# Performance work log

Hardware: AMD Instinct MI355X
Metric: run time of the kernel (lower is better)

Reference implementation:

```python
import jax, jax.numpy as jnp
import numpy as np

NUM_NODES = 10000
IN_DIM = 128
GAT_UNITS = 64
K = 20  # min(20, num_nodes - 1)
NEG_SLOPE = 0.2


def setup_inputs() -> dict:
    key = jax.random.key(0)
    ks = jax.random.split(key, 10)
    s = lambda k, shape, scale: jax.random.normal(k, shape, jnp.float32) * scale
    return {
        "x": s(ks[0], (NUM_NODES, IN_DIM), 1.0),
        "emb": s(ks[1], (NUM_NODES, 16), 1.0),
        "W1": s(ks[2], (IN_DIM, 4, GAT_UNITS), 0.05),
        "a1_src": s(ks[3], (4, GAT_UNITS), 0.05),
        "a1_tgt": s(ks[4], (4, GAT_UNITS), 0.05),
        "b1": jnp.zeros((4 * GAT_UNITS,), jnp.float32),
        "W2": s(ks[5], (4 * GAT_UNITS, 1, GAT_UNITS), 0.05),
        "a2_src": s(ks[6], (1, GAT_UNITS), 0.05),
        "a2_tgt": s(ks[7], (1, GAT_UNITS), 0.05),
        "b2": jnp.zeros((GAT_UNITS,), jnp.float32),
    }


def _build_edges(emb):
    # top-k adjacency from cosine similarity of node embeddings
    norm = emb / jnp.linalg.norm(emb, axis=-1, keepdims=True)
    sim = norm @ norm.T                      # [N, N]
    _, idx = jax.lax.top_k(sim, K)           # [N, K]
    n = emb.shape[0]
    src = jnp.repeat(jnp.arange(n, dtype=jnp.int32), K)
    tgt = idx.reshape(-1).astype(jnp.int32)
    # append self loops (as in the original module)
    loop = jnp.arange(n, dtype=jnp.int32)
    src = jnp.concatenate([src, loop])
    tgt = jnp.concatenate([tgt, loop])
    return src, tgt                          # each [N*(K+1)]


def _gat(x, W, a_src, a_tgt, src, tgt, n):
    # x: [N, F]; W: [F, H, C]; a_*: [H, C]
    h = jnp.einsum("nf,fhc->nhc", x, W)      # [N, H, C]
    e_src = jnp.einsum("nhc,hc->nh", h, a_src)  # [N, H]
    e_tgt = jnp.einsum("nhc,hc->nh", h, a_tgt)  # [N, H]
    logits = jax.nn.leaky_relu(e_src[src] + e_tgt[tgt], NEG_SLOPE)  # [E, H]
    # segment softmax over each source node's neighborhood
    m = jax.ops.segment_max(logits, src, num_segments=n)
    ex = jnp.exp(logits - m[src])
    z = jax.ops.segment_sum(ex, src, num_segments=n)
    alpha = ex / z[src]                      # [E, H]
    msg = alpha[:, :, None] * h[tgt]         # [E, H, C]
    return jax.ops.segment_sum(msg, src, num_segments=n)  # [N, H, C]


def reference(x, emb, W1, a1_src, a1_tgt, b1, W2, a2_src, a2_tgt, b2):
    n = x.shape[0]
    src, tgt = _build_edges(emb)
    # GAT layer 1: 4 heads, concatenated
    h1 = _gat(x, W1, a1_src, a1_tgt, src, tgt, n)        # [N, 4, C]
    h1 = h1.reshape(n, -1) + b1                           # [N, 4C]
    h1 = jax.nn.relu(h1)                                  # (dropout: inference mode)
    # GAT layer 2: 1 head, no concat
    h2 = _gat(h1, W2, a2_src, a2_tgt, src, tgt, n)        # [N, 1, C]
    return h2[:, 0, :] + b2                               # [N, C]
```

## Files before the change

### kernel.cpp

```cpp
#include <hip/hip_runtime.h>
#include <math.h>


#define N_NODES 10000
#define EMB_D   16
#define IN_DIM  128
#define H1      4
#define CDIM    64
#define D1      256
#define K_TOP   20
#define NEIGH   21
#define SROWS   32
#define NTILES  313
#define JSPLIT  2
#define HALFT   160
#define CAPM    96
#define GUARD   0.016f

typedef __attribute__((ext_vector_type(8)))  short short8;
typedef __attribute__((ext_vector_type(16))) float f32x16;

__device__ __forceinline__ unsigned monokey(float v) {
  unsigned u = __float_as_uint(v);
  return (u & 0x80000000u) ? ~u : (u | 0x80000000u);
}
__device__ __forceinline__ float invmono(unsigned m) {
  unsigned u = (m & 0x80000000u) ? (m ^ 0x80000000u) : ~m;
  return __uint_as_float(u);
}
__device__ __forceinline__ unsigned short f32_to_bf16(float f) {
  unsigned u = __float_as_uint(f);
  unsigned r = 0x7FFFu + ((u >> 16) & 1u);
  return (unsigned short)((u + r) >> 16);
}

__device__ __forceinline__ float dot16q(float4 qa, float4 qb, float4 qc, float4 qd,
                                        float4 v0, float4 v1, float4 v2, float4 v3) {
  float a = 0.f;
  a = fmaf(qa.x, v0.x, a); a = fmaf(qa.y, v0.y, a);
  a = fmaf(qa.z, v0.z, a); a = fmaf(qa.w, v0.w, a);
  a = fmaf(qb.x, v1.x, a); a = fmaf(qb.y, v1.y, a);
  a = fmaf(qb.z, v1.z, a); a = fmaf(qb.w, v1.w, a);
  a = fmaf(qc.x, v2.x, a); a = fmaf(qc.y, v2.y, a);
  a = fmaf(qc.z, v2.z, a); a = fmaf(qc.w, v2.w, a);
  a = fmaf(qd.x, v3.x, a); a = fmaf(qd.y, v3.y, a);
  a = fmaf(qd.z, v3.z, a); a = fmaf(qd.w, v3.w, a);
  return a;
}

__global__ __launch_bounds__(256) void normalize_kernel(
    const float* __restrict__ emb, float* __restrict__ nrm,
    unsigned short* __restrict__ nrmh) {
  int i = blockIdx.x * 256 + threadIdx.x;
  if (i >= N_NODES) return;
  const float4* p = (const float4*)(emb + (size_t)i * EMB_D);
  float4 v[4];
  float ss = 0.f;
#pragma unroll
  for (int k = 0; k < 4; k++) {
    v[k] = p[k];
    ss = fmaf(v[k].x, v[k].x, ss);
    ss = fmaf(v[k].y, v[k].y, ss);
    ss = fmaf(v[k].z, v[k].z, ss);
    ss = fmaf(v[k].w, v[k].w, ss);
  }
  float nv = sqrtf(ss);
  float4* o = (float4*)(nrm + (size_t)i * EMB_D);
  ushort4* oh = (ushort4*)(nrmh + (size_t)i * EMB_D);
#pragma unroll
  for (int k = 0; k < 4; k++) {
    float4 t;
    t.x = v[k].x / nv; t.y = v[k].y / nv; t.z = v[k].z / nv; t.w = v[k].w / nv;
    o[k] = t;
    ushort4 h;
    h.x = f32_to_bf16(t.x); h.y = f32_to_bf16(t.y);
    h.z = f32_to_bf16(t.z); h.w = f32_to_bf16(t.w);
    oh[k] = h;
  }
}

__global__ __launch_bounds__(512) void sim_topk_part(
    const float* __restrict__ nrm, const unsigned short* __restrict__ nrmh,
    unsigned long long* __restrict__ pkeys) {
  __shared__ unsigned short s_qbf[SROWS * EMB_D];
  __shared__ float s_qf[SROWS * EMB_D];
  __shared__ __align__(16) char s_ovl[32768];
  float (*s_smax)[256] = (float(*)[256])s_ovl;
  unsigned long long (*s_ckey)[CAPM] = (unsigned long long(*)[CAPM])s_ovl;
  unsigned short (*s_cid)[CAPM] =
      (unsigned short(*)[CAPM])(s_ovl + 24576);
  __shared__ float s_thr[SROWS];
  __shared__ int s_cnt[SROWS];

  int tid = threadIdx.x;
  int w = tid >> 6, lane = tid & 63;
  int lo5 = lane & 31, hi = lane >> 5;
  int row0 = blockIdx.x * SROWS;
  int bh = blockIdx.y;
  int tbase = bh * HALFT;

  if (tid < SROWS * EMB_D) {
    int gi = row0 * EMB_D + tid;
    float v = (gi < N_NODES * EMB_D) ? nrm[gi] : 0.f;
    s_qf[tid] = v;
    s_qbf[tid] = f32_to_bf16(v);
  }
  if (tid < SROWS) s_cnt[tid] = 0;
  __syncthreads();

  short8 afrag = *(const short8*)&s_qbf[lo5 * EMB_D + hi * 8];
  const f32x16 zacc = (f32x16)0.0f;

  float rm[16];
#pragma unroll
  for (int r = 0; r < 16; r++) rm[r] = -INFINITY;

#pragma unroll
  for (int g = 0; g < 5; ++g) {
    int tb = tbase + g * 32 + w * 4;
    int nd[4];
    short8 bf[4];
#pragma unroll
    for (int u = 0; u < 4; u++) {
      nd[u] = (tb + u) * 32 + lo5;
      bf[u] = (short8)(short)0;
      if (nd[u] < N_NODES)
        bf[u] = *(const short8*)&nrmh[(size_t)nd[u] * EMB_D + hi * 8];
    }
#pragma unroll
    for (int u = 0; u < 4; u++) {
      f32x16 acc = __builtin_amdgcn_mfma_f32_32x32x16_bf16(afrag, bf[u], zacc, 0, 0, 0);
      if (nd[u] < N_NODES) {
#pragma unroll
        for (int r = 0; r < 16; r++) rm[r] = fmaxf(rm[r], acc[r]);
      }
    }
  }
#pragma unroll
  for (int r = 0; r < 16; r++) {
    int rl = (r & 3) + 8 * (r >> 2) + 4 * hi;
    s_smax[rl][w * 32 + lo5] = rm[r];
  }
  __syncthreads();

  for (int q = 0; q < 4; q++) {
    int row = w * 4 + q;
    float m01 = fmaxf(s_smax[row][lane], s_smax[row][64 + lane]);
    float m23 = fmaxf(s_smax[row][128 + lane], s_smax[row][192 + lane]);
    unsigned v = monokey(fmaxf(m01, m23));
#pragma unroll
    for (int k = 2; k <= 64; k <<= 1) {
#pragma unroll
      for (int j = k >> 1; j > 0; j >>= 1) {
        unsigned o = __shfl_xor(v, j);
        bool upper = (lane & j) != 0;
        bool ascend = (lane & k) == 0;
        unsigned mx = v > o ? v : o;
        unsigned mn = v > o ? o : v;
        v = (upper == ascend) ? mx : mn;
      }
    }
    unsigned t20 = __shfl(v, 44);
    if (lane == 0)
      s_thr[row] = (row0 + row < N_NODES) ? invmono(t20) - GUARD : INFINITY;
  }
  __syncthreads();

  float thr_r[16];
#pragma unroll
  for (int r = 0; r < 16; r++)
    thr_r[r] = s_thr[(r & 3) + 8 * (r >> 2) + 4 * hi];

#pragma unroll
  for (int g = 0; g < 5; ++g) {
    int tb = tbase + g * 32 + w * 4;
    int nd[4];
    short8 bf[4];
#pragma unroll
    for (int u = 0; u < 4; u++) {
      nd[u] = (tb + u) * 32 + lo5;
      bf[u] = (short8)(short)0;
      if (nd[u] < N_NODES)
        bf[u] = *(const short8*)&nrmh[(size_t)nd[u] * EMB_D + hi * 8];
    }
#pragma unroll
    for (int u = 0; u < 4; u++) {
      f32x16 acc = __builtin_amdgcn_mfma_f32_32x32x16_bf16(afrag, bf[u], zacc, 0, 0, 0);
      if (nd[u] < N_NODES) {
#pragma unroll
        for (int r = 0; r < 16; r++) {
          if (acc[r] >= thr_r[r]) {
            int rl = (r & 3) + 8 * (r >> 2) + 4 * hi;
            int slot = atomicAdd(&s_cnt[rl], 1);
            if (slot < CAPM) s_cid[rl][slot] = (unsigned short)nd[u];
          }
        }
      }
    }
  }
  __syncthreads();

  for (int q = 0; q < 4; q++) {
    int row = w * 4 + q;
    if (row0 + row >= N_NODES) continue;
    int M = s_cnt[row];
    if (M > CAPM) continue;
    const float4* qp = (const float4*)&s_qf[row * EMB_D];
    float4 qa = qp[0], qb = qp[1], qc = qp[2], qd = qp[3];
    for (int c = lane; c < M; c += 64) {
      int id = s_cid[row][c];
      const float4* pj = (const float4*)(nrm + (size_t)id * EMB_D);
      float sim = dot16q(qa, qb, qc, qd, pj[0], pj[1], pj[2], pj[3]);
      s_ckey[row][c] = ((unsigned long long)monokey(sim) << 32) |
                       (unsigned long long)(0xFFFFFFFFu - (unsigned)id);
    }
  }
  __syncthreads();

  for (int q = 0; q < 4; q++) {
    int row = w * 4 + q;
    int grow = row0 + row;
    if (grow >= N_NODES) continue;
    unsigned long long* outp = pkeys + ((size_t)grow * JSPLIT + bh) * K_TOP;
    int M = s_cnt[row];
    if (M <= CAPM) {
      for (int c = lane; c < M; c += 64) {
        unsigned long long mykey = s_ckey[row][c];
        int rank = 0;
        for (int i = 0; i < M; i++) rank += (s_ckey[row][i] > mykey) ? 1 : 0;
        if (rank < K_TOP) outp[rank] = mykey;
      }
    } else {
      const float4* qp = (const float4*)&s_qf[row * EMB_D];
      float4 qa = qp[0], qb = qp[1], qc = qp[2], qd = qp[3];
      int j0 = tbase * 32;
      int jend = j0 + HALFT * 32; if (jend > N_NODES) jend = N_NODES;
      unsigned long long prev = ~0ull;
      for (int r = 0; r < K_TOP; r++) {
        unsigned long long best = 0ull;
        for (int j = j0 + lane; j < jend; j += 64) {
          const float4* pj = (const float4*)(nrm + (size_t)j * EMB_D);
          float sim = dot16q(qa, qb, qc, qd, pj[0], pj[1], pj[2], pj[3]);
          unsigned long long key = ((unsigned long long)monokey(sim) << 32) |
                                   (unsigned long long)(0xFFFFFFFFu - (unsigned)j);
          if (key < prev && key > best) best = key;
        }
#pragma unroll
        for (int off = 32; off > 0; off >>= 1) {
          unsigned long long o = __shfl_down(best, off);
          if (o > best) best = o;
        }
        best = __shfl(best, 0);
        prev = best;
        if (lane == 0) outp[r] = best;
      }
    }
  }
}

__global__ __launch_bounds__(256) void topk_merge(
    const unsigned long long* __restrict__ pkeys, int* __restrict__ topk) {
  __shared__ unsigned long long s_k[4][JSPLIT * K_TOP];
  int w = threadIdx.x >> 6, lane = threadIdx.x & 63;
  int row = blockIdx.x * 4 + w;
  const unsigned long long* src = pkeys + (size_t)row * (JSPLIT * K_TOP);
  if (lane < JSPLIT * K_TOP) s_k[w][lane] = src[lane];
  __syncthreads();
  if (lane < JSPLIT * K_TOP) {
    unsigned long long mykey = s_k[w][lane];
    int rank = 0;
    for (int i = 0; i < JSPLIT * K_TOP; i++)
      rank += (s_k[w][i] > mykey) ? 1 : 0;
    if (rank < K_TOP)
      topk[(size_t)row * K_TOP + rank] =
          (int)(0xFFFFFFFFu - (unsigned)(mykey & 0xFFFFFFFFull));
  }
}

__global__ __launch_bounds__(512) void gemm1_kernel(
    const float* __restrict__ A, const float* __restrict__ B,
    const float* __restrict__ a_src, const float* __restrict__ a_tgt,
    float* __restrict__ Cc, float* __restrict__ es, float* __restrict__ et) {
  __shared__ float As[16][IN_DIM];
  int r0 = blockIdx.x * 16;
  int tid = threadIdx.y * 256 + threadIdx.x;
  {
    int rr = tid >> 5;
    int kk = tid & 31;
    ((float4*)&As[rr][0])[kk] = ((const float4*)(A + (size_t)(r0 + rr) * IN_DIM))[kk];
  }
  __syncthreads();
  int col = threadIdx.x;
  int y = threadIdx.y;
  float acc[8] = {0, 0, 0, 0, 0, 0, 0, 0};
  for (int k4 = 0; k4 < IN_DIM / 4; k4++) {
    float4 a[8];
#pragma unroll
    for (int r = 0; r < 8; r++) a[r] = ((const float4*)&As[y * 8 + r][0])[k4];
    float bv[4];
#pragma unroll
    for (int i = 0; i < 4; i++) bv[i] = B[(size_t)(k4 * 4 + i) * D1 + col];
#pragma unroll
    for (int r = 0; r < 8; r++) {
      acc[r] = fmaf(a[r].x, bv[0], acc[r]);
      acc[r] = fmaf(a[r].y, bv[1], acc[r]);
      acc[r] = fmaf(a[r].z, bv[2], acc[r]);
      acc[r] = fmaf(a[r].w, bv[3], acc[r]);
    }
  }
#pragma unroll
  for (int r = 0; r < 8; r++)
    Cc[(size_t)(r0 + y * 8 + r) * D1 + col] = acc[r];
  float as = a_src[col], at = a_tgt[col];
  int h = col >> 6;
#pragma unroll
  for (int r = 0; r < 8; r++) {
    float ps = acc[r] * as, pt = acc[r] * at;
#pragma unroll
    for (int off = 32; off > 0; off >>= 1) {
      ps += __shfl_down(ps, off);
      pt += __shfl_down(pt, off);
    }
    if ((col & 63) == 0) {
      es[(size_t)(r0 + y * 8 + r) * H1 + h] = ps;
      et[(size_t)(r0 + y * 8 + r) * H1 + h] = pt;
    }
  }
}

__global__ __launch_bounds__(256) void agg1_gemm2_kernel(
    const float* __restrict__ h1p, const float* __restrict__ e1s,
    const float* __restrict__ e1t, const int* __restrict__ topk,
    const float* __restrict__ b1, const float* __restrict__ B2,
    const float* __restrict__ a_src, const float* __restrict__ a_tgt,
    float* __restrict__ h2p, float* __restrict__ es, float* __restrict__ et) {
  __shared__ float As[16][D1];
  __shared__ int nb[16][NEIGH];
  __shared__ float wv[16][NEIGH][H1];
  __shared__ float zz[16][H1];
  int r0 = blockIdx.x * 16;
  int tid = threadIdx.x;

  for (int idx = tid; idx < 16 * NEIGH; idx += 256) {
    int n = idx / NEIGH, jj = idx % NEIGH;
    nb[n][jj] = (jj < K_TOP) ? topk[(size_t)(r0 + n) * K_TOP + jj] : (r0 + n);
  }
  __syncthreads();
  for (int idx = tid; idx < 16 * NEIGH * H1; idx += 256) {
    int e = idx & 3, jj = (idx >> 2) % NEIGH, n = idx / (NEIGH * H1);
    float L = e1s[(size_t)(r0 + n) * H1 + e] + e1t[(size_t)nb[n][jj] * H1 + e];
    wv[n][jj][e] = (L > 0.f) ? L : 0.2f * L;
  }
  __syncthreads();
  if (tid < 16 * H1) {
    int n = tid >> 2, h = tid & 3;
    float m = -INFINITY;
#pragma unroll
    for (int jj = 0; jj < NEIGH; jj++) m = fmaxf(m, wv[n][jj][h]);
    float z = 0.f;
#pragma unroll
    for (int jj = 0; jj < NEIGH; jj++) {
      float wt = expf(wv[n][jj][h] - m);
      z += wt;
      wv[n][jj][h] = wt;
    }
    zz[n][h] = z;
  }
  __syncthreads();
  {
    int h = tid >> 6;
    float bv = b1[tid];
    for (int n = 0; n < 16; n++) {
      float acc = 0.f;
#pragma unroll
      for (int jj = 0; jj < NEIGH; jj++)
        acc = fmaf(wv[n][jj][h], h1p[(size_t)nb[n][jj] * D1 + tid], acc);
      float o = acc / zz[n][h] + bv;
      As[n][tid] = fmaxf(o, 0.f);
    }
  }
  __syncthreads();
  int col = tid & 63, y = tid >> 6;
  float acc4[4] = {0, 0, 0, 0};
  for (int k4 = 0; k4 < D1 / 4; k4++) {
    float4 a[4];
#pragma unroll
    for (int r = 0; r < 4; r++) a[r] = ((const float4*)&As[y * 4 + r][0])[k4];
    float bv[4];
#pragma unroll
    for (int i = 0; i < 4; i++) bv[i] = B2[(size_t)(k4 * 4 + i) * CDIM + col];
#pragma unroll
    for (int r = 0; r < 4; r++) {
      acc4[r] = fmaf(a[r].x, bv[0], acc4[r]);
      acc4[r] = fmaf(a[r].y, bv[1], acc4[r]);
      acc4[r] = fmaf(a[r].z, bv[2], acc4[r]);
      acc4[r] = fmaf(a[r].w, bv[3], acc4[r]);
    }
  }
#pragma unroll
  for (int r = 0; r < 4; r++)
    h2p[(size_t)(r0 + y * 4 + r) * CDIM + col] = acc4[r];
  float as = a_src[col], at = a_tgt[col];
#pragma unroll
  for (int r = 0; r < 4; r++) {
    float ps = acc4[r] * as, pt = acc4[r] * at;
#pragma unroll
    for (int off = 32; off > 0; off >>= 1) {
      ps += __shfl_down(ps, off);
      pt += __shfl_down(pt, off);
    }
    if (col == 0) {
      es[r0 + y * 4 + r] = ps;
      et[r0 + y * 4 + r] = pt;
    }
  }
}

__global__ __launch_bounds__(256) void agg2_kernel(
    const float* __restrict__ h2p, const float* __restrict__ es,
    const float* __restrict__ et, const int* __restrict__ topk,
    const float* __restrict__ b2, float* __restrict__ out) {
  int tid = threadIdx.x;
  int li = tid >> 6;
  int c = tid & 63;
  int i = blockIdx.x * 4 + li;
  __shared__ int nb[4][NEIGH];
  __shared__ float lg[4][NEIGH];
  if (tid < 4 * NEIGH) {
    int li2 = tid / NEIGH, jj = tid % NEIGH;
    int node = blockIdx.x * 4 + li2;
    nb[li2][jj] = (jj < K_TOP) ? topk[(size_t)node * K_TOP + jj] : node;
  }
  __syncthreads();
  if (tid < 4 * NEIGH) {
    int li2 = tid / NEIGH, jj = tid % NEIGH;
    int node = blockIdx.x * 4 + li2;
    float L = es[node] + et[nb[li2][jj]];
    lg[li2][jj] = (L > 0.f) ? L : 0.2f * L;
  }
  __syncthreads();
  float m = -INFINITY;
#pragma unroll
  for (int jj = 0; jj < NEIGH; jj++) m = fmaxf(m, lg[li][jj]);
  float z = 0.f, acc = 0.f;
#pragma unroll
  for (int jj = 0; jj < NEIGH; jj++) {
    float w = expf(lg[li][jj] - m);
    z += w;
    acc = fmaf(w, h2p[(size_t)nb[li][jj] * CDIM + c], acc);
  }
  out[(size_t)i * CDIM + c] = acc / z + b2[c];
}

extern "C" void kernel_launch(void* const* d_in, const int* in_sizes, int n_in,
                              void* d_out, int out_size, void* d_ws, size_t ws_size,
                              hipStream_t stream) {
  const float* x   = (const float*)d_in[0];
  const float* emb = (const float*)d_in[1];
  const float* W1  = (const float*)d_in[2];
  const float* a1s = (const float*)d_in[3];
  const float* a1t = (const float*)d_in[4];
  const float* b1  = (const float*)d_in[5];
  const float* W2  = (const float*)d_in[6];
  const float* a2s = (const float*)d_in[7];
  const float* a2t = (const float*)d_in[8];
  const float* b2  = (const float*)d_in[9];
  float* out = (float*)d_out;

  size_t off = 0;
  auto alloc = [&](size_t bytes) {
    void* p = (char*)d_ws + off;
    off += (bytes + 255) & ~(size_t)255;
    return p;
  };
  float*          nrm  = (float*)alloc((size_t)N_NODES * EMB_D * sizeof(float));
  unsigned short* nrmh = (unsigned short*)alloc((size_t)N_NODES * EMB_D * sizeof(unsigned short));
  int*   topk = (int*)  alloc((size_t)N_NODES * K_TOP * sizeof(int));
  float* h1p  = (float*)alloc((size_t)N_NODES * D1 * sizeof(float));
  float* e1s  = (float*)alloc((size_t)N_NODES * H1 * sizeof(float));
  float* e1t  = (float*)alloc((size_t)N_NODES * H1 * sizeof(float));
  float* h2p  = (float*)alloc((size_t)N_NODES * CDIM * sizeof(float));
  float* e2s  = (float*)alloc((size_t)N_NODES * sizeof(float));
  float* e2t  = (float*)alloc((size_t)N_NODES * sizeof(float));
  unsigned long long* pkeys = (unsigned long long*)h1p;
  (void)ws_size; (void)in_sizes; (void)n_in; (void)out_size;

  normalize_kernel<<<(N_NODES + 255) / 256, 256, 0, stream>>>(emb, nrm, nrmh);
  sim_topk_part<<<dim3(NTILES, JSPLIT), 512, 0, stream>>>(nrm, nrmh, pkeys);
  topk_merge<<<N_NODES / 4, 256, 0, stream>>>(pkeys, topk);
  gemm1_kernel<<<N_NODES / 16, dim3(256, 2), 0, stream>>>(x, W1, a1s, a1t, h1p, e1s, e1t);
  agg1_gemm2_kernel<<<N_NODES / 16, 256, 0, stream>>>(h1p, e1s, e1t, topk, b1,
                                                      W2, a2s, a2t, h2p, e2s, e2t);
  agg2_kernel<<<N_NODES / 4, 256, 0, stream>>>(h2p, e2s, e2t, topk, b2, out);
}
```

Baseline: 146.1 us.

## Use wavefront bitonic sort for small candidate sets and 2-column gemm1 threads

```diff
diff --git a/kernel.cpp b/kernel.cpp
--- a/kernel.cpp
+++ b/kernel.cpp
@@ -223,7 +223,22 @@
     if (grow >= N_NODES) continue;
     unsigned long long* outp = pkeys + ((size_t)grow * JSPLIT + bh) * K_TOP;
     int M = s_cnt[row];
-    if (M <= CAPM) {
+    if (M <= 64) {
+      unsigned long long key = (lane < M) ? s_ckey[row][lane] : 0ull;
+#pragma unroll
+      for (int k = 2; k <= 64; k <<= 1) {
+#pragma unroll
+        for (int j = k >> 1; j > 0; j >>= 1) {
+          unsigned long long o = __shfl_xor(key, j);
+          bool upper = (lane & j) != 0;
+          bool ascend = (lane & k) == 0;
+          unsigned long long mx = key > o ? key : o;
+          unsigned long long mn = key > o ? o : key;
+          key = (upper == ascend) ? mx : mn;
+        }
+      }
+      if (lane >= 64 - K_TOP) outp[63 - lane] = key;
+    } else if (M <= CAPM) {
       for (int c = lane; c < M; c += 64) {
         unsigned long long mykey = s_ckey[row][c];
         int rank = 0;
@@ -277,51 +292,63 @@
   }
 }
 
-__global__ __launch_bounds__(512) void gemm1_kernel(
+__global__ __launch_bounds__(256) void gemm1_kernel(
     const float* __restrict__ A, const float* __restrict__ B,
     const float* __restrict__ a_src, const float* __restrict__ a_tgt,
     float* __restrict__ Cc, float* __restrict__ es, float* __restrict__ et) {
   __shared__ float As[16][IN_DIM];
   int r0 = blockIdx.x * 16;
-  int tid = threadIdx.y * 256 + threadIdx.x;
+  int tid = threadIdx.x;
   {
-    int rr = tid >> 5;
-    int kk = tid & 31;
+    int rr = tid >> 4;
+    int kk = tid & 15;
     ((float4*)&As[rr][0])[kk] = ((const float4*)(A + (size_t)(r0 + rr) * IN_DIM))[kk];
-  }
-  __syncthreads();
-  int col = threadIdx.x;
-  int y = threadIdx.y;
-  float acc[8] = {0, 0, 0, 0, 0, 0, 0, 0};
+    ((float4*)&As[rr][0])[kk + 16] =
+        ((const float4*)(A + (size_t)(r0 + rr) * IN_DIM))[kk + 16];
+  }
+  __syncthreads();
+  int y = tid >> 7;
+  int c0 = (tid & 127) * 2;
+  float acc[8][2] = {};
   for (int k4 = 0; k4 < IN_DIM / 4; k4++) {
     float4 a[8];
 #pragma unroll
     for (int r = 0; r < 8; r++) a[r] = ((const float4*)&As[y * 8 + r][0])[k4];
-    float bv[4];
-#pragma unroll
-    for (int i = 0; i < 4; i++) bv[i] = B[(size_t)(k4 * 4 + i) * D1 + col];
+    float2 bv[4];
+#pragma unroll
+    for (int i = 0; i < 4; i++)
+      bv[i] = *(const float2*)&B[(size_t)(k4 * 4 + i) * D1 + c0];
 #pragma unroll
     for (int r = 0; r < 8; r++) {
-      acc[r] = fmaf(a[r].x, bv[0], acc[r]);
-      acc[r] = fmaf(a[r].y, bv[1], acc[r]);
-      acc[r] = fmaf(a[r].z, bv[2], acc[r]);
-      acc[r] = fmaf(a[r].w, bv[3], acc[r]);
-    }
-  }
-#pragma unroll
-  for (int r = 0; r < 8; r++)
-    Cc[(size_t)(r0 + y * 8 + r) * D1 + col] = acc[r];
-  float as = a_src[col], at = a_tgt[col];
-  int h = col >> 6;
+      acc[r][0] = fmaf(a[r].x, bv[0].x, acc[r][0]);
+      acc[r][1] = fmaf(a[r].x, bv[0].y, acc[r][1]);
+      acc[r][0] = fmaf(a[r].y, bv[1].x, acc[r][0]);
+      acc[r][1] = fmaf(a[r].y, bv[1].y, acc[r][1]);
+      acc[r][0] = fmaf(a[r].z, bv[2].x, acc[r][0]);
+      acc[r][1] = fmaf(a[r].z, bv[2].y, acc[r][1]);
+      acc[r][0] = fmaf(a[r].w, bv[3].x, acc[r][0]);
+      acc[r][1] = fmaf(a[r].w, bv[3].y, acc[r][1]);
+    }
+  }
 #pragma unroll
   for (int r = 0; r < 8; r++) {
-    float ps = acc[r] * as, pt = acc[r] * at;
-#pragma unroll
-    for (int off = 32; off > 0; off >>= 1) {
+    float2 o = {acc[r][0], acc[r][1]};
+    *(float2*)&Cc[(size_t)(r0 + y * 8 + r) * D1 + c0] = o;
+  }
+  int lane = tid & 63;
+  int h = c0 >> 6;
+  float as0 = a_src[c0], as1 = a_src[c0 + 1];
+  float at0 = a_tgt[c0], at1 = a_tgt[c0 + 1];
+#pragma unroll
+  for (int r = 0; r < 8; r++) {
+    float ps = fmaf(acc[r][1], as1, acc[r][0] * as0);
+    float pt = fmaf(acc[r][1], at1, acc[r][0] * at0);
+#pragma unroll
+    for (int off = 16; off > 0; off >>= 1) {
       ps += __shfl_down(ps, off);
       pt += __shfl_down(pt, off);
     }
-    if ((col & 63) == 0) {
+    if ((lane & 31) == 0) {
       es[(size_t)(r0 + y * 8 + r) * H1 + h] = ps;
       et[(size_t)(r0 + y * 8 + r) * H1 + h] = pt;
     }
@@ -488,7 +515,7 @@
   normalize_kernel<<<(N_NODES + 255) / 256, 256, 0, stream>>>(emb, nrm, nrmh);
   sim_topk_part<<<dim3(NTILES, JSPLIT), 512, 0, stream>>>(nrm, nrmh, pkeys);
   topk_merge<<<N_NODES / 4, 256, 0, stream>>>(pkeys, topk);
-  gemm1_kernel<<<N_NODES / 16, dim3(256, 2), 0, stream>>>(x, W1, a1s, a1t, h1p, e1s, e1t);
+  gemm1_kernel<<<N_NODES / 16, 256, 0, stream>>>(x, W1, a1s, a1t, h1p, e1s, e1t);
   agg1_gemm2_kernel<<<N_NODES / 16, 256, 0, stream>>>(h1p, e1s, e1t, topk, b1,
                                                       W2, a2s, a2t, h2p, e2s, e2t);
   agg2_kernel<<<N_NODES / 4, 256, 0, stream>>>(h2p, e2s, e2t, topk, b2, out);
```

Result: no change. 144.1 us (-1.3%).
